# Kernel tuning notes

Measured on AMD Instinct MI355X. Metric: run time of the kernel, lower is better.

The kernel has to match this reference:

```python
import jax, jax.numpy as jnp
import numpy as np

NMS_THRESH = 0.4          # used as both iou_threshold and score_threshold (as in source)
VAR0, VAR1 = 0.1, 0.2     # variances
MAX_OUT = 200             # max_output_size hardcoded in source
N_ANCHORS = 172032        # 2*(256^2+128^2+64^2), strides 8/16/32 on 2048x2048


def _decode(cls_pred, reg_pred, lnd_pred, anchors):
    # scores: prob of face class (column 1)
    scores = cls_pred.reshape(-1, 2)[:, 1]
    reg = reg_pred.reshape(-1, 4) * jnp.array([VAR0, VAR0, VAR1, VAR1], dtype=reg_pred.dtype)
    dx, dy, dw, dh = reg[:, 0], reg[:, 1], reg[:, 2], reg[:, 3]
    x_a, y_a, w_a, h_a = anchors[:, 0], anchors[:, 1], anchors[:, 2], anchors[:, 3]
    xc = dx * w_a + x_a
    yc = dy * h_a + y_a
    w = jnp.exp(dw) * w_a
    h = jnp.exp(dh) * h_a
    # boxes in [ymin, xmin, ymax, xmax] (tf.image.non_max_suppression convention)
    boxes = jnp.stack([yc - h / 2, xc - w / 2, yc + h / 2, xc + w / 2], axis=1)
    lnd = lnd_pred.reshape(-1, 5, 2) * VAR0
    lx = lnd[..., 0] * w_a[:, None] + x_a[:, None]
    ly = lnd[..., 1] * h_a[:, None] + y_a[:, None]
    lnd10 = jnp.stack([lx, ly], axis=-1).reshape(-1, 10)
    return boxes, scores, lnd10


def _nms(boxes, scores):
    # Greedy NMS, fixed MAX_OUT iterations; invalid slots flagged False.
    y1, x1, y2, x2 = boxes[:, 0], boxes[:, 1], boxes[:, 2], boxes[:, 3]
    areas = (y2 - y1) * (x2 - x1)
    s0 = jnp.where(scores > NMS_THRESH, scores, -jnp.inf)  # score_threshold

    def step(s, _):
        i = jnp.argmax(s)
        valid = s[i] > -jnp.inf
        b = boxes[i]  # (4,) = [iy1, ix1, iy2, ix2]
        ih = jnp.maximum(jnp.minimum(y2, b[2]) - jnp.maximum(y1, b[0]), 0.0)
        iw = jnp.maximum(jnp.minimum(x2, b[3]) - jnp.maximum(x1, b[1]), 0.0)
        inter = ih * iw
        iou = inter / (areas + areas[i] - inter + 1e-12)
        # selected box has IoU 1 with itself -> suppressed too
        s = jnp.where(valid & (iou > NMS_THRESH), -jnp.inf, s)
        return s, (i, valid)

    _, (idxs, valids) = jax.lax.scan(step, s0, None, length=MAX_OUT)
    return idxs, valids


def setup_inputs() -> dict:
    key = jax.random.key(0)
    k1, k2, k3, k4 = jax.random.split(key, 4)
    N = N_ANCHORS
    cls_pred = jax.random.normal(k1, (N, 2), jnp.float32)
    reg_pred = jax.random.normal(k2, (N, 4), jnp.float32) * 0.5
    lnd_pred = jax.random.normal(k3, (N, 10), jnp.float32) * 0.5
    centers = jax.random.uniform(k4, (N, 2), jnp.float32)  # normalized anchor centers
    wh = jnp.full((N, 2), 0.05, jnp.float32)               # anchor widths/heights
    anchors = jnp.concatenate([centers, wh], axis=1)       # [N,4] = (xc, yc, w, h)
    return {"cls_pred": cls_pred, "reg_pred": reg_pred, "lnd_pred": lnd_pred, "anchors": anchors}


def reference(cls_pred, reg_pred, lnd_pred, anchors):
    boxes, scores, lnd10 = _decode(cls_pred, reg_pred, lnd_pred, anchors)
    idxs, valids = _nms(boxes, scores)
    m = valids.astype(boxes.dtype)[:, None]
    # fixed-shape padded outputs: invalid rows zeroed (tf returns variable length)
    return boxes[idxs] * m, lnd10[idxs] * m
```

## Files before the change

kernel.cpp:

```cpp
#include <hip/hip_runtime.h>
#include <stdint.h>

#pragma clang fp contract(off)

#define N_ANCHORS 172032
#define MAX_OUT 200
#define BLK 1024
#define GRID 168
#define NW (BLK / 64)
#define SEG 32
#define NKEY (GRID * SEG)
#define RMAX 1024
#define MASKW (RMAX / 64)
#define RCAND 64
#define RGRID (NKEY / RCAND)
#define RBLK 512
#define RW (RBLK / 64)
#define MGRID 64
#define VT 2.35f

typedef unsigned long long ull;
static_assert(GRID * BLK == N_ANCHORS, "grid covers anchors exactly");
static_assert(RMAX % 64 == 0, "mask words");
static_assert(RGRID * RCAND == NKEY, "rank grid covers key capacity");
static_assert(GRID <= 192, "prefix scan uses 3 waves");

__device__ __forceinline__ void decode_box_d(const float4* __restrict__ reg,
                                             const float4* __restrict__ anc, int i,
                                             double b[4]) {
#pragma clang fp contract(off)
    float4 r = reg[i];
    float4 a = anc[i];
    double dx = (double)r.x * 0.1;
    double dy = (double)r.y * 0.1;
    double dw = (double)r.z * 0.2;
    double dh = (double)r.w * 0.2;
    double xa = (double)a.x, ya = (double)a.y, wa = (double)a.z, ha = (double)a.w;
    double xc = dx * wa; xc = xc + xa;
    double yc = dy * ha; yc = yc + ya;
    double w = exp(dw) * wa;
    double h = exp(dh) * ha;
    double h2 = h * 0.5, w2 = w * 0.5;
    b[0] = yc - h2; b[1] = xc - w2; b[2] = yc + h2; b[3] = xc + w2;
}

__device__ __forceinline__ void write_row(const float4* __restrict__ reg,
                                          const float4* __restrict__ anc,
                                          const float* __restrict__ lnd,
                                          int q, int idx, float* __restrict__ out) {
#pragma clang fp contract(off)
    float4 bv = make_float4(0.f, 0.f, 0.f, 0.f);
    float2 lv[5];
    for (int j = 0; j < 5; ++j) lv[j] = make_float2(0.f, 0.f);
    if (idx >= 0) {
        double bb[4];
        decode_box_d(reg, anc, idx, bb);
        bv = make_float4((float)bb[0], (float)bb[1], (float)bb[2], (float)bb[3]);
        float4 a = anc[idx];
        double xa = (double)a.x, ya = (double)a.y, wa = (double)a.z, ha = (double)a.w;
        const float2* l2p = (const float2*)lnd;
        for (int j = 0; j < 5; ++j) {
            float2 lp = l2p[idx * 5 + j];
            double lx = (double)lp.x * 0.1;
            double ly = (double)lp.y * 0.1;
            lx = lx * wa; lx = lx + xa;
            ly = ly * ha; ly = ly + ya;
            lv[j] = make_float2((float)lx, (float)ly);
        }
    }
    *(float4*)&out[q * 4] = bv;
    float2* o2 = (float2*)&out[MAX_OUT * 4 + q * 10];
    for (int j = 0; j < 5; ++j) o2[j] = lv[j];
}

__device__ __forceinline__ ull wmax(ull k) {
    for (int d = 32; d > 0; d >>= 1) {
        ull o = __shfl_down(k, d, 64);
        if (o > k) k = o;
    }
    return k;
}

__device__ __forceinline__ ull readlane64(ull v, int l) {
    unsigned lo = (unsigned)__builtin_amdgcn_readlane((int)(unsigned)(v & 0xffffffffull), l);
    unsigned hi = (unsigned)__builtin_amdgcn_readlane((int)(unsigned)(v >> 32), l);
    return ((ull)hi << 32) | (ull)lo;
}

__device__ __forceinline__ bool iou_gt_f4(float4 a, float4 p) {
#pragma clang fp contract(off)
    double y1 = (double)a.x, x1 = (double)a.y, y2 = (double)a.z, x2 = (double)a.w;
    double p0 = (double)p.x, p1 = (double)p.y, p2 = (double)p.z, p3 = (double)p.w;
    double ih = fmin(y2, p2) - fmax(y1, p0); ih = fmax(ih, 0.0);
    double iw = fmin(x2, p3) - fmax(x1, p1); iw = fmax(iw, 0.0);
    double inter = ih * iw;
    double aj = (y2 - y1) * (x2 - x1);
    double ap = (p2 - p0) * (p3 - p1);
    double den = aj + ap; den = den - inter; den = den + 1e-12;
    return (inter / den) > 0.4;
}

__global__ void __launch_bounds__(BLK) k_seg(const float2* __restrict__ cls,
                                             int* __restrict__ segcnt,
                                             ull* __restrict__ segkeys,
                                             int* __restrict__ cnt) {
    __shared__ int wcnt[NW];
    int tid = threadIdx.x, bid = blockIdx.x;
    if (bid == 0 && tid == 0) cnt[0] = 0;
    int i = bid * BLK + tid;
    float sc = cls[i].y;
    bool c = (sc > VT);
    ull key = 0ull;
    if (c) key = ((ull)__float_as_uint(sc) << 32)
               | (ull)(0xFFFFFFFFu - (unsigned int)i);
    ull m = __ballot(c);
    int wid = tid >> 6, lane = tid & 63;
    if (lane == 0) wcnt[wid] = __popcll(m);
    __syncthreads();
    if (tid == 0) {
        int s = 0;
        for (int w = 0; w < NW; ++w) { int t = wcnt[w]; wcnt[w] = s; s += t; }
        segcnt[bid] = s;
    }
    __syncthreads();
    if (c) {
        int pos = wcnt[wid] + __popcll(m & ((1ull << lane) - 1ull));
        if (pos < SEG) segkeys[bid * SEG + pos] = key;
    }
}

__device__ __forceinline__ void rank_emit(const float4* __restrict__ reg,
                                          const float4* __restrict__ anc,
                                          int rank, ull key,
                                          int* __restrict__ gidx,
                                          float4* __restrict__ gbox) {
    int idx = (int)(0xFFFFFFFFu - (unsigned int)key);
    gidx[rank] = idx;
    double b[4];
    decode_box_d(reg, anc, idx, b);
    gbox[rank] = make_float4((float)b[0], (float)b[1], (float)b[2], (float)b[3]);
}

__global__ void __launch_bounds__(RBLK) k_rank(const float4* __restrict__ reg,
                                               const float4* __restrict__ anc,
                                               const int* __restrict__ segcnt,
                                               const ull* __restrict__ segkeys,
                                               int* __restrict__ meta,
                                               int* __restrict__ gidx,
                                               float4* __restrict__ gbox) {
    __shared__ ull skeys[NKEY];
    __shared__ int scnt[GRID], spre[GRID];
    __shared__ int wsum[4];
    __shared__ ull wovf[4];
    __shared__ int spart[RBLK];
    __shared__ int s_ok, s_csel;
    int tid = threadIdx.x, wid = tid >> 6, lane = tid & 63;

    int v = 0; bool ovf = false;
    if (tid < GRID) { v = segcnt[tid]; scnt[tid] = v; ovf = (v > SEG); }
    int x = v;
    for (int d = 1; d < 64; d <<= 1) {
        int o = __shfl_up(x, d, 64);
        if (lane >= d) x += o;
    }
    ull om = __ballot(ovf);
    if (wid < 3 && lane == 63) { wsum[wid] = x; wovf[wid] = om; }
    __syncthreads();
    if (tid == 0) {
        int total = wsum[0] + wsum[1] + wsum[2];
        s_csel = total;
        s_ok = ((wovf[0] | wovf[1] | wovf[2]) == 0ull) ? 1 : 0;
        if (blockIdx.x == 0) { meta[0] = s_ok; meta[1] = total; }
    }
    __syncthreads();
    if (tid < GRID)
        spre[tid] = (x - v) + (wid >= 1 ? wsum[0] : 0) + (wid >= 2 ? wsum[1] : 0);
    bool okl = (s_ok != 0);
    int csel = s_csel;
    int cbase = blockIdx.x * RCAND;
    __syncthreads();
    if (!okl) return;
    if (cbase >= csel) return;

    for (int t = tid; t < GRID * SEG; t += RBLK) {
        int s = t >> 5, k = t & (SEG - 1);
        if (k < scnt[s]) skeys[spre[s] + k] = segkeys[t];
    }
    __syncthreads();

    int per = (csel + RW - 1) / RW;
    int jb = wid * per;
    int je = jb + per; if (je > csel) je = csel;
    int c = cbase + lane;
    ull kc = (c < csel) ? skeys[c] : 0ull;
    int rk = 0;
#pragma unroll 8
    for (int j = jb; j < je; ++j)
        rk += (skeys[j] > kc) ? 1 : 0;
    spart[wid * 64 + lane] = rk;
    __syncthreads();

    if (tid < RCAND) {
        int cc = cbase + tid;
        if (cc < csel) {
            int r = 0;
#pragma unroll
            for (int w = 0; w < RW; ++w) r += spart[w * 64 + tid];
            if (r < RMAX) rank_emit(reg, anc, r, skeys[cc], gidx, gbox);
        }
    }
}

__global__ void __launch_bounds__(BLK) k_mp(const float2* __restrict__ cls,
                                            const float4* __restrict__ reg,
                                            const float4* __restrict__ anc,
                                            const float* __restrict__ lnd,
                                            const int* __restrict__ meta,
                                            const int* __restrict__ gidx,
                                            const float4* __restrict__ gbox,
                                            ull* __restrict__ gmask,
                                            int* __restrict__ cnt,
                                            float* __restrict__ sbuf,
                                            float* __restrict__ out) {
    __shared__ union {
        float4 cbox[RMAX];
        __align__(16) ull smask[RMAX * MASKW];
    } u;
    __shared__ int s_kept[MAX_OUT];
    __shared__ int s_ln, s_last;
    __shared__ ull warr[NW];
    __shared__ ull s_win;
    __shared__ double s_pb[5];

    int tid = threadIdx.x, bid = blockIdx.x;
    int wid = tid >> 6, lane = tid & 63;
    bool pre_ok = (meta[0] != 0);
    int csel = meta[1];
    int rlim = csel < RMAX ? csel : RMAX;

    if (pre_ok && rlim > 0) {
        for (int t = tid; t < rlim; t += BLK) u.cbox[t] = gbox[t];
        __syncthreads();
        int totw = rlim * MASKW;
        for (int w = bid * NW + wid; w < totw; w += MGRID * NW) {
            int row = w >> 4, word = w & (MASKW - 1);
            int col = (word << 6) + lane;
            bool hit = (col < rlim) && iou_gt_f4(u.cbox[col], u.cbox[row]);
            ull bits = __ballot(hit);
            if (lane == 0) gmask[w] = bits;
        }
    }
    __syncthreads();
    if (tid == 0) {
        __threadfence();
        int prev = atomicAdd(cnt, 1);
        s_last = (prev == MGRID - 1) ? 1 : 0;
    }
    __syncthreads();
    if (!s_last) return;
    __threadfence();

    int ln = 0;
    if (pre_ok) {
        int nv4 = rlim * (MASKW / 2);
        const float4* gm4 = (const float4*)gmask;
        float4* sm4 = (float4*)u.smask;
        for (int t = tid; t < nv4; t += BLK) sm4[t] = gm4[t];
        __syncthreads();
        if (tid < 64) {
            ull alive = 0ull;
            if (lane < MASKW) {
                int lo = lane << 6;
                int n = rlim - lo;
                if (n >= 64) alive = ~0ull;
                else if (n > 0) alive = (1ull << n) - 1ull;
            }
            int lnl = 0;
            while (lnl < MAX_OUT) {
                ull bal = __ballot(alive != 0ull);
                if (bal == 0ull) break;
                int wl = __ffsll(bal) - 1;
                ull aw = readlane64(alive, wl);
                int bit = __ffsll(aw) - 1;
                int p = (wl << 6) + bit;
                if (lane == 0) s_kept[lnl] = p;
                lnl++;
                ull rw = (lane < MASKW) ? u.smask[p * MASKW + lane] : 0ull;
                alive &= ~rw;
            }
            if (lane == 0) s_ln = lnl;
        }
        __syncthreads();
        ln = s_ln;
    }

    bool need = (!pre_ok) || (ln < MAX_OUT);
    if (!need) {
        if (tid < MAX_OUT) write_row(reg, anc, lnd, tid, gidx[s_kept[tid]], out);
        return;
    }

    for (int i = tid; i < N_ANCHORS; i += BLK) {
        float sc = cls[i].y;
        sbuf[i] = ((double)sc > 0.4) ? sc : 0.0f;
    }
    __syncthreads();
    ln = 0;
    for (int oi = 0; oi < MAX_OUT; ++oi) {
        ull k = 0;
        for (int i = tid; i < N_ANCHORS; i += BLK) {
            ull kk = ((ull)__float_as_uint(sbuf[i]) << 32)
                   | (ull)(0xFFFFFFFFu - (unsigned int)i);
            if (kk > k) k = kk;
        }
        k = wmax(k);
        if ((tid & 63) == 0) warr[tid >> 6] = k;
        __syncthreads();
        if (tid < 64) {
            ull v = (tid < NW) ? warr[tid] : 0ull;
            v = wmax(v);
            if (tid == 0) s_win = v;
        }
        __syncthreads();
        ull win = s_win;
        if ((win >> 32) == 0u) break;
        int pidx = (int)(0xFFFFFFFFu - (unsigned int)win);
        if (tid == 0) {
            double b[4];
            decode_box_d(reg, anc, pidx, b);
            s_pb[0] = b[0]; s_pb[1] = b[1]; s_pb[2] = b[2]; s_pb[3] = b[3];
            s_pb[4] = (b[2] - b[0]) * (b[3] - b[1]);
            s_kept[oi] = pidx;
        }
        __syncthreads();
        double p0 = s_pb[0], p1 = s_pb[1], p2 = s_pb[2], p3 = s_pb[3], pa = s_pb[4];
        for (int i = tid; i < N_ANCHORS; i += BLK) {
            float v = sbuf[i];
            if (v != 0.0f) {
                double b[4];
                decode_box_d(reg, anc, i, b);
                double ih = fmin(b[2], p2) - fmax(b[0], p0); ih = fmax(ih, 0.0);
                double iw = fmin(b[3], p3) - fmax(b[1], p1); iw = fmax(iw, 0.0);
                double inter = ih * iw;
                double aa = (b[2] - b[0]) * (b[3] - b[1]);
                double den = aa + pa; den = den - inter; den = den + 1e-12;
                if (inter / den > 0.4) sbuf[i] = 0.0f;
            }
        }
        __syncthreads();
        ln = oi + 1;
    }
    __syncthreads();
    if (tid < MAX_OUT)
        write_row(reg, anc, lnd, tid, (tid < ln) ? s_kept[tid] : -1, out);
}

extern "C" void kernel_launch(void* const* d_in, const int* in_sizes, int n_in,
                              void* d_out, int out_size, void* d_ws, size_t ws_size,
                              hipStream_t stream) {
    const float2* cls = (const float2*)d_in[0];
    const float4* reg = (const float4*)d_in[1];
    const float*  lnd = (const float*)d_in[2];
    const float4* anc = (const float4*)d_in[3];

    uint8_t* w = (uint8_t*)d_ws;
    int*    segcnt  = (int*)w;
    int*    meta    = (int*)(w + 768);
    int*    cnt     = (int*)(w + 896);
    ull*    segkeys = (ull*)(w + 1024);
    int*    gidx    = (int*)(w + 44032);
    float4* gbox    = (float4*)(w + 48128);
    ull*    gmask   = (ull*)(w + 64512);
    float*  sbuf    = (float*)(w + 44032);

    k_seg <<<GRID, BLK, 0, stream>>>(cls, segcnt, segkeys, cnt);
    k_rank<<<RGRID, RBLK, 0, stream>>>(reg, anc, segcnt, segkeys, meta, gidx, gbox);
    k_mp  <<<MGRID, BLK, 0, stream>>>(cls, reg, anc, lnd, meta, gidx, gbox, gmask,
                                      cnt, sbuf, (float*)d_out);
}
```

Measured before the change: 115.7 us.

## Process NMS mask chunk-wise with diagonal resolution and batched row OR

Restructures the serial greedy scan over the precomputed suppression bitmask into 64-candidate chunks. Within a chunk, the keeps are resolved using only the chunk's diagonal mask words, read through lane-local registers with readlane. The kept rows' masks are then OR-reduced in parallel: four lane groups each take up to eight rows per pass, and the groups are combined with xor-shuffles. This replaces one dependent LDS load plus ballot per kept box with mostly register operations, in exchange for more complex control flow.

```diff
diff --git a/kernel.cpp b/kernel.cpp
--- a/kernel.cpp
+++ b/kernel.cpp
@@ -87,6 +87,12 @@
     return ((ull)hi << 32) | (ull)lo;
 }
 
+__device__ __forceinline__ ull shflx64(ull v, int m) {
+    int lo = __shfl_xor((int)(unsigned)(v & 0xffffffffull), m, 64);
+    int hi = __shfl_xor((int)(unsigned)(v >> 32), m, 64);
+    return ((ull)(unsigned)hi << 32) | (ull)(unsigned)lo;
+}
+
 __device__ __forceinline__ bool iou_gt_f4(float4 a, float4 p) {
 #pragma clang fp contract(off)
     double y1 = (double)a.x, x1 = (double)a.y, y2 = (double)a.z, x2 = (double)a.w;
@@ -276,17 +282,45 @@
                 else if (n > 0) alive = (1ull << n) - 1ull;
             }
             int lnl = 0;
-            while (lnl < MAX_OUT) {
-                ull bal = __ballot(alive != 0ull);
-                if (bal == 0ull) break;
-                int wl = __ffsll(bal) - 1;
-                ull aw = readlane64(alive, wl);
-                int bit = __ffsll(aw) - 1;
-                int p = (wl << 6) + bit;
-                if (lane == 0) s_kept[lnl] = p;
-                lnl++;
-                ull rw = (lane < MASKW) ? u.smask[p * MASKW + lane] : 0ull;
-                alive &= ~rw;
+            int nchunk = (rlim + 63) >> 6;
+            int g = lane >> 4, w = lane & 15;
+            for (int c = 0; c < nchunk && lnl < MAX_OUT; ++c) {
+                ull aw = readlane64(alive, c);
+                if (aw == 0ull) continue;
+                int rowid = (c << 6) + lane;
+                ull diag = (rowid < rlim) ? u.smask[rowid * MASKW + c] : 0ull;
+                ull cur = aw, pmask = 0ull;
+                while (cur != 0ull && lnl < MAX_OUT) {
+                    int b = __ffsll(cur) - 1;
+                    if (lane == 0) s_kept[lnl] = (c << 6) + b;
+                    lnl++;
+                    pmask |= (1ull << b);
+                    ull rowb = readlane64(diag, b);
+                    cur &= ~rowb;
+                }
+                if (lnl >= MAX_OUT) break;
+                ull pm = pmask;
+                ull supp0 = 0ull, supp1 = 0ull;
+                while (pm != 0ull) {
+                    int b0 = __ffsll(pm) - 1; pm &= pm - 1ull;
+                    int b1 = b0, b2 = b0, b3 = b0, b4 = b0, b5 = b0, b6 = b0, b7 = b0;
+                    if (pm) { b1 = __ffsll(pm) - 1; pm &= pm - 1ull; }
+                    if (pm) { b2 = __ffsll(pm) - 1; pm &= pm - 1ull; }
+                    if (pm) { b3 = __ffsll(pm) - 1; pm &= pm - 1ull; }
+                    if (pm) { b4 = __ffsll(pm) - 1; pm &= pm - 1ull; }
+                    if (pm) { b5 = __ffsll(pm) - 1; pm &= pm - 1ull; }
+                    if (pm) { b6 = __ffsll(pm) - 1; pm &= pm - 1ull; }
+                    if (pm) { b7 = __ffsll(pm) - 1; pm &= pm - 1ull; }
+                    int bg0 = (g == 0) ? b0 : (g == 1) ? b1 : (g == 2) ? b2 : b3;
+                    int bg1 = (g == 0) ? b4 : (g == 1) ? b5 : (g == 2) ? b6 : b7;
+                    ull rw0 = u.smask[((c << 6) + bg0) * MASKW + w];
+                    ull rw1 = u.smask[((c << 6) + bg1) * MASKW + w];
+                    supp0 |= rw0; supp1 |= rw1;
+                }
+                ull supp = supp0 | supp1;
+                supp |= shflx64(supp, 16);
+                supp |= shflx64(supp, 32);
+                alive &= ~supp;
             }
             if (lane == 0) s_ln = lnl;
         }
```

Measured after the change: 113.6 us. About the same (-1.8%).
